# Kernel optimization log

Measured on AMD Instinct MI355X. Metric: run time of the kernel, lower is better.

## Reference

```python
import jax, jax.numpy as jnp
import numpy as np

B, S, D = 32, 2048, 1024
COS_EPS = 1e-8  # torch CosineSimilarity default eps (module's self.eps is unused)


def setup_inputs() -> dict:
    key = jax.random.key(0)
    ks = jax.random.split(key, 7)
    k = jax.random.normal(ks[0], (B, D), dtype=jnp.float32)
    xs = jax.random.normal(ks[1], (B, S, D), dtype=jnp.float32)
    mask = jnp.ones((B, S), dtype=bool)
    Wa = jax.random.normal(ks[2], (D, D), dtype=jnp.float32) / np.sqrt(D)
    Wb = jax.random.normal(ks[3], (D, D), dtype=jnp.float32) / np.sqrt(D)
    energy = jax.random.normal(ks[4], (D,), dtype=jnp.float32)
    Wc = jax.random.normal(ks[5], (D, 2 * D), dtype=jnp.float32) / np.sqrt(2 * D)
    bc = jax.random.normal(ks[6], (D,), dtype=jnp.float32) * 0.01
    return {"k": k, "xs": xs, "mask": mask, "Wa": Wa, "Wb": Wb,
            "energy": energy, "Wc": Wc, "bc": bc}


def _masked_softmax(scores, mask):
    scores = jnp.where(mask, scores, -jnp.inf)
    return jax.nn.softmax(scores, axis=-1)


def reference(k, xs, mask, Wa, Wb, energy, Wc, bc):
    # --- cosine-similarity attention ---
    k_n = k / jnp.maximum(jnp.linalg.norm(k, axis=-1, keepdims=True), COS_EPS)      # [B,D]
    xs_n = xs / jnp.maximum(jnp.linalg.norm(xs, axis=-1, keepdims=True), COS_EPS)   # [B,S,D]
    cos_sim = jnp.einsum('bd,bsd->bs', k_n, xs_n)                                    # [B,S]
    a_cos = _masked_softmax(cos_sim, mask)
    cos_repr = jnp.einsum('bs,bsd->bd', a_cos, xs)

    # --- Bahdanau (additive) attention ---
    # Wa(k) broadcast over seq instead of repeat; Linear is x @ W.T
    wk = k @ Wa.T                                                                     # [B,D]
    wx = jnp.einsum('bsd,ed->bse', xs, Wb)                                            # [B,S,D]
    w = jnp.tanh(wk[:, None, :] + wx) @ energy                                        # [B,S]
    a_bah = _masked_softmax(w, mask)
    bah_repr = jnp.einsum('bs,bsd->bd', a_bah, xs)

    # --- combine ---
    attn = jnp.concatenate([cos_repr, bah_repr], axis=-1) @ Wc.T + bc                 # [B,D]
    atts = (a_cos + a_bah) * 0.5                                                      # [B,S]
    return attn, atts
```

## Files before the change

### kernel.cpp

```cpp
#include <hip/hip_runtime.h>
#include <math.h>

#define NB 32
#define NS 2048
#define ND 1024
#define NM (NB*NS)
#define KT 32

typedef __attribute__((ext_vector_type(4))) float f32x4;
typedef __attribute__((ext_vector_type(8))) _Float16 f16x8;
typedef __attribute__((ext_vector_type(4))) _Float16 f16x4;
typedef unsigned short u16;

__device__ __forceinline__ void gload_lds16(const void* g, void* l) {
  __builtin_amdgcn_global_load_lds(
      (const __attribute__((address_space(1))) void*)g,
      (__attribute__((address_space(3))) void*)l, 16, 0, 0);
}

__global__ void k2_setup(const float* __restrict__ xs, const float* __restrict__ k,
                         float* __restrict__ norm2, float* __restrict__ dotk,
                         u16* __restrict__ XsF,
                         const float* __restrict__ Wb, u16* __restrict__ WbF,
                         float* __restrict__ knorm,
                         const float* __restrict__ Wa, float* __restrict__ wk,
                         float* __restrict__ wacc, float* __restrict__ crep,
                         float* __restrict__ brep) {
  const int bx = blockIdx.x;
  const int t = threadIdx.x;
  if (bx < 2048) {
    const int lane = t & 63;
    const int w = t >> 6;
    const int base = bx * 32 + w * 8;
#pragma unroll 1
    for (int r = 0; r < 8; ++r) {
      const int row = base + r;
      const int bb = row >> 11;
      const float* xr = xs + (size_t)row * ND;
      const float* kr = k + (size_t)bb * ND;
      float n2 = 0.f, dk = 0.f;
#pragma unroll
      for (int p = 0; p < 4; ++p) {
        const int d = (p * 64 + lane) * 4;
        f32x4 x = *(const f32x4*)(xr + d);
        f32x4 kv = *(const f32x4*)(kr + d);
        union { _Float16 a[4]; unsigned long long v; } F;
#pragma unroll
        for (int j = 0; j < 4; ++j) {
          n2 += x[j] * x[j]; dk += x[j] * kv[j];
          F.a[j] = (_Float16)x[j];
        }
        *(unsigned long long*)(XsF + (size_t)row * ND + d) = F.v;
      }
      for (int off = 32; off >= 1; off >>= 1) { n2 += __shfl_xor(n2, off); dk += __shfl_xor(dk, off); }
      if (lane == 0) { norm2[row] = n2; dotk[row] = dk; }
    }
  } else if (bx < 3072) {
    int i = ((bx - 2048) * 256 + t) * 4;
    f32x4 x = *(const f32x4*)(Wb + i);
    union { _Float16 a[4]; unsigned long long v; } F;
#pragma unroll
    for (int j = 0; j < 4; ++j) F.a[j] = (_Float16)x[j];
    *(unsigned long long*)(WbF + i) = F.v;
  } else if (bx < 3104) {
    int b = bx - 3072;
    float s = 0.f;
    for (int d = t; d < ND; d += 256) { float v = k[b * ND + d]; s += v * v; }
    for (int off = 32; off >= 1; off >>= 1) s += __shfl_xor(s, off);
    __shared__ float lds[4];
    int lane = t & 63, wid = t >> 6;
    if (lane == 0) lds[wid] = s;
    __syncthreads();
    if (t == 0) knorm[b] = sqrtf(lds[0] + lds[1] + lds[2] + lds[3]);
  } else if (bx < 3232) {
    int g = (bx - 3104) * 256 + t;
    int b = g & 31;
    int e = g >> 5;
    const float* kr = k + b * ND;
    const float* wr = Wa + (size_t)e * ND;
    float s = 0.f;
    for (int d = 0; d < ND; d += 4) {
      f32x4 a = *(const f32x4*)(kr + d);
      f32x4 w = *(const f32x4*)(wr + d);
      s += a[0] * w[0] + a[1] * w[1] + a[2] * w[2] + a[3] * w[3];
    }
    wk[b * ND + e] = s;
  } else {
    int g = (bx - 3232) * 256 + t;
    if (g < NM) wacc[g] = 0.f;
    if (g < NB * ND) { crep[g] = 0.f; brep[g] = 0.f; }
  }
}

#define MFMA(a, bb, d) d = __builtin_amdgcn_mfma_f32_16x16x32_f16(a, bb, d, 0, 0, 0)
#define SB0 __builtin_amdgcn_sched_barrier(0)

#define MFMA_PASS(A, row) \
  MFMA(A, b0, acc[row][0]); MFMA(A, b1, acc[row][1]); \
  MFMA(A, b2, acc[row][2]); MFMA(A, b3, acc[row][3]);

#define G8(S, p) \
  __builtin_amdgcn_s_setprio(1); \
  MFMA_PASS(S##0, 2*(p)); \
  MFMA_PASS(S##1, 2*(p)+1); \
  __builtin_amdgcn_s_setprio(0);

#define READ_SET(S, base, p) \
  S##0 = *(const f16x8*)((base) + aOff + (2*(p))*512); \
  S##1 = *(const f16x8*)((base) + aOff + (2*(p)+1)*512);

#define READ_B4(src) \
  b0 = *(const f16x8*)((src) + bOff + 0*512); \
  b1 = *(const f16x8*)((src) + bOff + 1*512); \
  b2 = *(const f16x8*)((src) + bOff + 2*512); \
  b3 = *(const f16x8*)((src) + bOff + 3*512);

__global__ __launch_bounds__(512, 4) void k4_gemm(
    const u16* __restrict__ XsF, const u16* __restrict__ WbF,
    const float* __restrict__ wk, const float* __restrict__ energy,
    float* __restrict__ wacc) {
  __shared__ u16 lds[32768];

  const int tid = threadIdx.x;
  const int bid = blockIdx.x;
  const int nt = bid & 7;
  const int mt = bid >> 3;
  const int lane = tid & 63;
  const int wid = tid >> 6;
  const int wm = wid >> 1, wn = wid & 1;
  const int l15 = lane & 15, kg = lane >> 4;

  const int sr = tid >> 2, sslot = tid & 3;
  const int scol = ((sslot ^ ((sr >> 1) & 3)) << 3);
  const size_t aRow0 = (size_t)(mt * 256 + sr) * ND;
  const size_t aRow1 = aRow0 + (size_t)128 * ND;
  const size_t bRow0 = (size_t)(nt * 128 + sr) * ND;

  const int fswz = (kg ^ ((l15 >> 1) & 3)) << 3;
  const int aOff = (wm * 64 + l15) * 32 + fswz;
  const int bOff = (wn * 64 + l15) * 32 + fswz;

  f32x4 acc[4][4] = {};
  f16x8 b0, b1, b2, b3;
  f16x8 s00, s01;
  f16x8 s10, s11;

  auto stageA = [&](int kcol, u16* dst) {
    gload_lds16(XsF + aRow0 + kcol + scol, dst);
    gload_lds16(XsF + aRow1 + kcol + scol, dst + 4096);
  };
  auto stageB = [&](int kcol, u16* dst) {
    gload_lds16(WbF + bRow0 + kcol + scol, dst);
  };

  stageA(0, lds + tid * 8);
  stageB(0, lds + 24576 + tid * 8);
  stageA(32, lds + 8192 + tid * 8);
  asm volatile("s_waitcnt vmcnt(2)" ::: "memory");
  __builtin_amdgcn_s_barrier();

  const u16* As  = lds;
  const u16* AsN = lds + 8192;
  u16*       AsW = lds + 16384;
  const u16* Bs  = lds + 24576;
  u16*       BsW = lds + 28672;

  READ_B4(Bs);
  READ_SET(s0, As, 0);

#pragma unroll 1
  for (int t = 0; t < KT; ++t) {
    const int kb = (t + 1 < KT ? t + 1 : KT - 1) * 32;
    const int ka = (t + 2 < KT ? t + 2 : KT - 1) * 32;

    stageB(kb, BsW + tid * 8);
    READ_SET(s1, As, 1);
    G8(s0, 0);
    stageA(ka, AsW + tid * 8);
    G8(s1, 1);
    asm volatile("s_waitcnt vmcnt(2)" ::: "memory");
    __builtin_amdgcn_s_barrier();
    SB0;
    READ_B4((const u16*)BsW);
    READ_SET(s0, AsN, 0);
    u16* tA = (u16*)As; As = AsN; AsN = AsW; AsW = tA;
    u16* tB = (u16*)Bs; Bs = (const u16*)BsW; BsW = tB;
  }
  asm volatile("s_waitcnt vmcnt(0)" ::: "memory");

  const int b = mt >> 3;
  const float* wkrow = wk + b * ND;
  const int ebase = nt * 128 + wn * 64 + l15;
  float wkv[4], env[4];
#pragma unroll
  for (int nf = 0; nf < 4; ++nf) { wkv[nf] = wkrow[ebase + nf * 16]; env[nf] = energy[ebase + nf * 16]; }
  const int rowOut = mt * 256 + wm * 64 + kg * 4;
#pragma unroll
  for (int mf = 0; mf < 4; ++mf) {
#pragma unroll
    for (int j = 0; j < 4; ++j) {
      float s = 0.f;
#pragma unroll
      for (int nf = 0; nf < 4; ++nf) s += tanhf(wkv[nf] + acc[mf][nf][j]) * env[nf];
      s += __shfl_xor(s, 1); s += __shfl_xor(s, 2);
      s += __shfl_xor(s, 4); s += __shfl_xor(s, 8);
      if (l15 == 0) atomicAdd(&wacc[rowOut + mf * 16 + j], s);
    }
  }
}

__global__ void k5_softmax(const float* __restrict__ wacc, const float* __restrict__ dotk,
                           const float* __restrict__ norm2, const float* __restrict__ knorm,
                           float* __restrict__ a_cos, float* __restrict__ a_bah,
                           float* __restrict__ out) {
  const int b = blockIdx.x;
  const int t = threadIdx.x;
  const int lane = t & 63, wid = t >> 6;
  __shared__ float lm1[4], lm2[4], ls1[4], ls2[4];
  const float kn = fmaxf(knorm[b], 1e-8f);
  float cs[8], wv[8];
  float mc = -1e30f, mw = -1e30f;
#pragma unroll
  for (int i = 0; i < 8; ++i) {
    size_t idx = (size_t)b * NS + i * 256 + t;
    float xn = fmaxf(sqrtf(norm2[idx]), 1e-8f);
    cs[i] = dotk[idx] / (kn * xn);
    wv[i] = wacc[idx];
    mc = fmaxf(mc, cs[i]); mw = fmaxf(mw, wv[i]);
  }
  for (int off = 32; off >= 1; off >>= 1) { mc = fmaxf(mc, __shfl_xor(mc, off)); mw = fmaxf(mw, __shfl_xor(mw, off)); }
  if (lane == 0) { lm1[wid] = mc; lm2[wid] = mw; }
  __syncthreads();
  mc = fmaxf(fmaxf(lm1[0], lm1[1]), fmaxf(lm1[2], lm1[3]));
  mw = fmaxf(fmaxf(lm2[0], lm2[1]), fmaxf(lm2[2], lm2[3]));
  float sc = 0.f, sw = 0.f;
#pragma unroll
  for (int i = 0; i < 8; ++i) {
    cs[i] = expf(cs[i] - mc); wv[i] = expf(wv[i] - mw);
    sc += cs[i]; sw += wv[i];
  }
  for (int off = 32; off >= 1; off >>= 1) { sc += __shfl_xor(sc, off); sw += __shfl_xor(sw, off); }
  if (lane == 0) { ls1[wid] = sc; ls2[wid] = sw; }
  __syncthreads();
  sc = ls1[0] + ls1[1] + ls1[2] + ls1[3];
  sw = ls2[0] + ls2[1] + ls2[2] + ls2[3];
  const float rc = 1.f / sc, rw = 1.f / sw;
#pragma unroll
  for (int i = 0; i < 8; ++i) {
    size_t idx = (size_t)b * NS + i * 256 + t;
    float ac = cs[i] * rc, ab = wv[i] * rw;
    a_cos[idx] = ac; a_bah[idx] = ab;
    out[NB * ND + idx] = 0.5f * (ac + ab);
  }
}

__global__ void k6_wsum(const u16* __restrict__ XsF, const float* __restrict__ a_cos,
                        const float* __restrict__ a_bah,
                        float* __restrict__ crep, float* __restrict__ brep) {
  const int b = blockIdx.y;
  const int s0 = blockIdx.x * 128;
  const int t = threadIdx.x;
  const int d0 = t * 4;
  f32x4 aC = {0.f, 0.f, 0.f, 0.f};
  f32x4 aB = {0.f, 0.f, 0.f, 0.f};
  for (int i = 0; i < 128; ++i) {
    size_t ridx = (size_t)b * NS + s0 + i;
    float ac = a_cos[ridx], ab = a_bah[ridx];
    f16x4 h = *(const f16x4*)(XsF + ridx * ND + d0);
#pragma unroll
    for (int j = 0; j < 4; ++j) {
      float x = (float)h[j];
      aC[j] += ac * x;
      aB[j] += ab * x;
    }
  }
#pragma unroll
  for (int j = 0; j < 4; ++j) {
    atomicAdd(&crep[b * ND + d0 + j], aC[j]);
    atomicAdd(&brep[b * ND + d0 + j], aB[j]);
  }
}

__global__ void k7_final(const float* __restrict__ crep, const float* __restrict__ brep,
                         const float* __restrict__ Wc, const float* __restrict__ bc,
                         float* __restrict__ out) {
  const int e = blockIdx.x;
  const int t = threadIdx.x;
  const int lane = t & 63, wid = t >> 6;
  const float* wr = Wc + (size_t)e * 2048;
  for (int bi = 0; bi < 8; ++bi) {
    const int b = wid * 8 + bi;
    float s = 0.f;
    for (int d = lane; d < 1024; d += 64) s += crep[b * ND + d] * wr[d];
    for (int d = lane; d < 1024; d += 64) s += brep[b * ND + d] * wr[1024 + d];
    for (int off = 32; off >= 1; off >>= 1) s += __shfl_xor(s, off);
    if (lane == 0) out[b * ND + e] = s + bc[e];
  }
}

extern "C" void kernel_launch(void* const* d_in, const int* in_sizes, int n_in,
                              void* d_out, int out_size, void* d_ws, size_t ws_size,
                              hipStream_t stream) {
  (void)in_sizes; (void)n_in; (void)out_size; (void)ws_size;
  const float* k      = (const float*)d_in[0];
  const float* xs     = (const float*)d_in[1];
  const float* Wa     = (const float*)d_in[3];
  const float* Wb     = (const float*)d_in[4];
  const float* energy = (const float*)d_in[5];
  const float* Wc     = (const float*)d_in[6];
  const float* bcv    = (const float*)d_in[7];
  float* out = (float*)d_out;

  char* w = (char*)d_ws;
  u16* XsF   = (u16*)w; w += (size_t)NM * ND * 2;
  u16* WbF   = (u16*)w; w += (size_t)1024 * 1024 * 2;
  float* wkbuf = (float*)w; w += (size_t)32 * 1024 * 4;
  float* norm2 = (float*)w; w += (size_t)NM * 4;
  float* dotk  = (float*)w; w += (size_t)NM * 4;
  float* wacc  = (float*)w; w += (size_t)NM * 4;
  float* a_cos = (float*)w; w += (size_t)NM * 4;
  float* a_bah = (float*)w; w += (size_t)NM * 4;
  float* crep  = (float*)w; w += (size_t)32 * 1024 * 4;
  float* brep  = (float*)w; w += (size_t)32 * 1024 * 4;
  float* knorm = (float*)w; w += 256;

  k2_setup<<<dim3(3488), dim3(256), 0, stream>>>(xs, k, norm2, dotk, XsF,
                                                 Wb, WbF, knorm, Wa, wkbuf,
                                                 wacc, crep, brep);
  k4_gemm<<<dim3(2048), dim3(512), 0, stream>>>(XsF, WbF, wkbuf, energy, wacc);
  k5_softmax<<<dim3(32), dim3(256), 0, stream>>>(wacc, dotk, norm2, knorm, a_cos, a_bah, out);
  k6_wsum<<<dim3(16, 32), dim3(256), 0, stream>>>(XsF, a_cos, a_bah, crep, brep);
  k7_final<<<dim3(1024), dim3(256), 0, stream>>>(crep, brep, Wc, bcv, out);
}
```

Baseline: 436.5 us.

## Widen setup row loads and remap GEMM tiles for XCD-local reuse

The setup kernel now gives each 32-lane half-wave one row and issues all eight 16-byte loads per thread up front, replacing the serial 8-row loop per wave. The grid grows from 3488 to 9632 blocks to cover this. This raises memory-level parallelism in the fp32-to-fp16 conversion pass, which is bandwidth bound. Separately, the GEMM block index is remapped so each XCD handles a contiguous set of 32 M-tiles across all N-tiles, aiming to keep A-tile reuse within one XCD's L2. The risks are higher register use and more block scheduling overhead.

```diff
diff --git a/kernel.cpp b/kernel.cpp
--- a/kernel.cpp
+++ b/kernel.cpp
@@ -28,42 +28,40 @@
                          float* __restrict__ brep) {
   const int bx = blockIdx.x;
   const int t = threadIdx.x;
-  if (bx < 2048) {
-    const int lane = t & 63;
-    const int w = t >> 6;
-    const int base = bx * 32 + w * 8;
-#pragma unroll 1
-    for (int r = 0; r < 8; ++r) {
-      const int row = base + r;
-      const int bb = row >> 11;
-      const float* xr = xs + (size_t)row * ND;
-      const float* kr = k + (size_t)bb * ND;
-      float n2 = 0.f, dk = 0.f;
-#pragma unroll
-      for (int p = 0; p < 4; ++p) {
-        const int d = (p * 64 + lane) * 4;
-        f32x4 x = *(const f32x4*)(xr + d);
-        f32x4 kv = *(const f32x4*)(kr + d);
-        union { _Float16 a[4]; unsigned long long v; } F;
-#pragma unroll
-        for (int j = 0; j < 4; ++j) {
-          n2 += x[j] * x[j]; dk += x[j] * kv[j];
-          F.a[j] = (_Float16)x[j];
-        }
-        *(unsigned long long*)(XsF + (size_t)row * ND + d) = F.v;
+  if (bx < 8192) {
+    const int sub = t & 31;
+    const int row = bx * 8 + (t >> 5);
+    const int bb = row >> 11;
+    const float* xr = xs + (size_t)row * ND;
+    const float* kr = k + (size_t)bb * ND;
+    f32x4 xv[8], kv[8];
+#pragma unroll
+    for (int c = 0; c < 8; ++c) xv[c] = *(const f32x4*)(xr + c * 128 + sub * 4);
+#pragma unroll
+    for (int c = 0; c < 8; ++c) kv[c] = *(const f32x4*)(kr + c * 128 + sub * 4);
+    float n2 = 0.f, dk = 0.f;
+#pragma unroll
+    for (int c = 0; c < 8; ++c) {
+      union { _Float16 a[4]; unsigned long long v; } F;
+#pragma unroll
+      for (int j = 0; j < 4; ++j) {
+        n2 += xv[c][j] * xv[c][j];
+        dk += xv[c][j] * kv[c][j];
+        F.a[j] = (_Float16)xv[c][j];
       }
-      for (int off = 32; off >= 1; off >>= 1) { n2 += __shfl_xor(n2, off); dk += __shfl_xor(dk, off); }
-      if (lane == 0) { norm2[row] = n2; dotk[row] = dk; }
+      *(unsigned long long*)(XsF + (size_t)row * ND + c * 128 + sub * 4) = F.v;
     }
-  } else if (bx < 3072) {
-    int i = ((bx - 2048) * 256 + t) * 4;
+    for (int off = 16; off >= 1; off >>= 1) { n2 += __shfl_xor(n2, off); dk += __shfl_xor(dk, off); }
+    if (sub == 0) { norm2[row] = n2; dotk[row] = dk; }
+  } else if (bx < 9216) {
+    int i = ((bx - 8192) * 256 + t) * 4;
     f32x4 x = *(const f32x4*)(Wb + i);
     union { _Float16 a[4]; unsigned long long v; } F;
 #pragma unroll
     for (int j = 0; j < 4; ++j) F.a[j] = (_Float16)x[j];
     *(unsigned long long*)(WbF + i) = F.v;
-  } else if (bx < 3104) {
-    int b = bx - 3072;
+  } else if (bx < 9248) {
+    int b = bx - 9216;
     float s = 0.f;
     for (int d = t; d < ND; d += 256) { float v = k[b * ND + d]; s += v * v; }
     for (int off = 32; off >= 1; off >>= 1) s += __shfl_xor(s, off);
@@ -72,8 +70,8 @@
     if (lane == 0) lds[wid] = s;
     __syncthreads();
     if (t == 0) knorm[b] = sqrtf(lds[0] + lds[1] + lds[2] + lds[3]);
-  } else if (bx < 3232) {
-    int g = (bx - 3104) * 256 + t;
+  } else if (bx < 9376) {
+    int g = (bx - 9248) * 256 + t;
     int b = g & 31;
     int e = g >> 5;
     const float* kr = k + b * ND;
@@ -86,7 +84,7 @@
     }
     wk[b * ND + e] = s;
   } else {
-    int g = (bx - 3232) * 256 + t;
+    int g = (bx - 9376) * 256 + t;
     if (g < NM) wacc[g] = 0.f;
     if (g < NB * ND) { crep[g] = 0.f; brep[g] = 0.f; }
   }
@@ -123,8 +121,10 @@
 
   const int tid = threadIdx.x;
   const int bid = blockIdx.x;
-  const int nt = bid & 7;
-  const int mt = bid >> 3;
+  const int xcd = bid & 7;
+  const int local = bid >> 3;
+  const int nt = local >> 5;
+  const int mt = xcd * 32 + (local & 31);
   const int lane = tid & 63;
   const int wid = tid >> 6;
   const int wm = wid >> 1, wn = wid & 1;
@@ -324,7 +324,7 @@
   float* brep  = (float*)w; w += (size_t)32 * 1024 * 4;
   float* knorm = (float*)w; w += 256;
 
-  k2_setup<<<dim3(3488), dim3(256), 0, stream>>>(xs, k, norm2, dotk, XsF,
+  k2_setup<<<dim3(9632), dim3(256), 0, stream>>>(xs, k, norm2, dotk, XsF,
                                                  Wb, WbF, knorm, Wa, wkbuf,
                                                  wacc, crep, brep);
   k4_gemm<<<dim3(2048), dim3(512), 0, stream>>>(XsF, WbF, wkbuf, energy, wacc);
```

Measured after the change: 435.4 us. Within noise of the previous version (-0.2%).
